# Optimization experiments

Measured on AMD Instinct MI355X. Metric: run time of the kernel, lower is better.

Reference implementation:

```python
import jax, jax.numpy as jnp
import numpy as np

N_NODES = 50000
N_EDGES = 800000
IN_DIM = 128
OUT_DIM = 128
NUM_RELS = 100
NUM_BASES = 4


def setup_inputs() -> dict:
    key = jax.random.key(0)
    ks = jax.random.split(key, 8)
    h = jax.random.normal(ks[0], (N_NODES, IN_DIM), dtype=jnp.float32)
    norm = jax.random.uniform(ks[1], (N_NODES, 1), dtype=jnp.float32)
    src = jax.random.randint(ks[2], (N_EDGES,), 0, N_NODES, dtype=jnp.int32)
    dst = jax.random.randint(ks[3], (N_EDGES,), 0, N_NODES, dtype=jnp.int32)
    rel_type = jax.random.randint(ks[4], (N_EDGES,), 0, NUM_RELS, dtype=jnp.int32)
    basis_weights = jax.random.normal(ks[5], (NUM_BASES, IN_DIM, OUT_DIM), dtype=jnp.float32) * (2.0 / np.sqrt(IN_DIM + OUT_DIM))
    coefficients = jax.random.normal(ks[6], (NUM_RELS, NUM_BASES), dtype=jnp.float32) * (1.0 / np.sqrt(NUM_RELS + NUM_BASES))
    loop_weight = jax.random.normal(ks[7], (IN_DIM, OUT_DIM), dtype=jnp.float32) * (2.0 / np.sqrt(IN_DIM + OUT_DIM))
    return {
        'h': h, 'norm': norm, 'src': src, 'dst': dst, 'rel_type': rel_type,
        'basis_weights': basis_weights, 'coefficients': coefficients,
        'loop_weight': loop_weight,
    }


def reference(h, norm, src, dst, rel_type, basis_weights, coefficients, loop_weight):
    # h: (N, in), norm: (N, 1), src/dst/rel_type: (E,)
    # basis_weights: (B, in, out), coefficients: (R, B), loop_weight: (in, out)
    n_nodes = h.shape[0]
    num_bases = basis_weights.shape[0]

    # self-loop message (dropout=0 -> identity)
    loop_message = h @ loop_weight  # (N, out)

    # W[r] = sum_b coeff[r, b] * basis[b]; per-edge msg_e = h[src_e] @ W[rel_e].
    # Reassociated: project nodes by each basis once, then mix per edge by
    # the relation coefficients -- identical math, avoids the (E, in, out)
    # gathered weight tensor of the original per-edge bmm.
    hb = jnp.einsum('ni,bio->bno', h, basis_weights)  # (B, N, out)
    c_e = coefficients[rel_type]  # (E, B)
    msg = c_e[:, 0, None] * hb[0][src]
    for b in range(1, num_bases):  # small fixed basis count
        msg = msg + c_e[:, b, None] * hb[b][src]  # (E, out)

    # scatter-sum aggregation to destination nodes, then norm scaling
    agg = jax.ops.segment_sum(msg, dst, num_segments=n_nodes)  # (N, out)
    node_repr = agg * norm  # _apply_func
    node_repr = node_repr + loop_message  # self-loop (bias=None)
    return jax.nn.relu(node_repr)  # activation
```

## Files before the change

kernel.cpp:

```cpp
#include <hip/hip_runtime.h>

typedef short bf16x8 __attribute__((ext_vector_type(8)));
typedef float floatx4 __attribute__((ext_vector_type(4)));
typedef float floatx2 __attribute__((ext_vector_type(2)));

typedef const __attribute__((address_space(1))) void* gas_ptr;
typedef __attribute__((address_space(3))) void* las_ptr;

#define EPB  4096
#define MAXB 6144

__device__ __forceinline__ unsigned short f2bf(float f) {
    unsigned int u = __float_as_uint(f);
    unsigned int r = u + 0x7fffu + ((u >> 16) & 1u);
    return (unsigned short)(r >> 16);
}

__device__ __forceinline__ void stage16(const void* g, void* lbase, int lane) {
#if __has_builtin(__builtin_amdgcn_global_load_lds)
    __builtin_amdgcn_global_load_lds((gas_ptr)g, (las_ptr)lbase, 16, 0, 0);
#else
    *(float4*)((char*)lbase + lane * 16) = *(const float4*)g;
#endif
}

__global__ __launch_bounds__(256) void prep_all(
    const float* __restrict__ h, unsigned short* __restrict__ hbf, int nconv,
    const int* __restrict__ dst, int* __restrict__ gh, int E, int nB, int nblkH,
    const float* __restrict__ basis, const float* __restrict__ loopw,
    unsigned short* __restrict__ WT2, int nb_conv)
{
    __shared__ int lh[256];
    const int b = blockIdx.x;
    const int t = threadIdx.x;
    if (b < nb_conv) {
        int idx = b * 256 + t;
        if (idx < nconv) {
            float2 v = *(const float2*)(h + (size_t)idx * 2);
            unsigned int pack = (unsigned int)f2bf(v.x) | ((unsigned int)f2bf(v.y) << 16);
            *(unsigned int*)(hbf + (size_t)idx * 2) = pack;
        }
    } else if (b < nb_conv + nblkH) {
        const int blk = b - nb_conv;
        lh[t] = 0;
        __syncthreads();
        const int cbase = blk * EPB;
#pragma unroll
        for (int j = 0; j < EPB / 256; ++j) {
            int e = cbase + j * 256 + t;
            if (e < E) atomicAdd(&lh[dst[e] >> 8], 1);
        }
        __syncthreads();
        if (t < nB) gh[(size_t)t * nblkH + blk] = lh[t];
    } else {
        int c = b - nb_conv - nblkH;
        for (int k = t; k < 640; k += 256) {
            float v;
            if (k < 512) v = basis[(size_t)k * 128 + c];
            else         v = loopw[(size_t)(k - 512) * 128 + c];
            WT2[(size_t)c * 640 + k] = f2bf(v);
        }
    }
}

__global__ __launch_bounds__(256) void scatter_bkt(
    const int* __restrict__ dst, const int* __restrict__ src,
    const int* __restrict__ rel, const int* __restrict__ gh,
    int* __restrict__ binStart, unsigned int* __restrict__ tmp,
    int E, int nB, int nblkH)
{
    __shared__ int ss[256];
    __shared__ int cur[256];
    const int j = blockIdx.x;
    const int t = threadIdx.x;

    int pre = 0, tot = 0;
    if (t < nB) {
        const int* row = gh + (size_t)t * nblkH;
#pragma unroll 8
        for (int c = 0; c < nblkH; ++c) {
            int v = row[c];
            tot += v;
            if (c < j) pre += v;
        }
    }
    int v = (t < nB) ? tot : 0;
    ss[t] = v;
    __syncthreads();
    for (int o = 1; o < 256; o <<= 1) {
        int x = (t >= o) ? ss[t - o] : 0;
        __syncthreads();
        ss[t] += x;
        __syncthreads();
    }
    const int gstart = ss[t] - v;
    cur[t] = gstart + pre;
    if (j == 0) {
        if (t < nB) binStart[t] = gstart;
        if (t == 0) binStart[nB] = E;
    }
    __syncthreads();

    const int cbase = j * EPB;
#pragma unroll
    for (int jj = 0; jj < EPB / 256; ++jj) {
        int e = cbase + jj * 256 + t;
        if (e < E) {
            int d = dst[e];
            int slot = atomicAdd(&cur[d >> 8], 1);
            tmp[slot] = (unsigned int)src[e] | ((unsigned int)rel[e] << 16)
                      | ((unsigned int)(d & 255) << 23);
        }
    }
}

__global__ __launch_bounds__(256) void bucket_sort(
    const unsigned int* __restrict__ tmp, const int* __restrict__ binStart,
    unsigned int* __restrict__ sedge, int* __restrict__ rowptr,
    int E, int N, int nB)
{
    __shared__ unsigned int eb[MAXB];
    __shared__ int hh[256], ss[256], cur[256];
    const int b = blockIdx.x;
    const int t = threadIdx.x;
    const int brow = binStart[b];
    const int next = binStart[b + 1];
    int n = next - brow;
    if (n > MAXB) n = MAXB;
    hh[t] = 0;
    __syncthreads();
    for (int i = t; i < n; i += 256) {
        unsigned int v = tmp[brow + i];
        eb[i] = v;
        atomicAdd(&hh[(v >> 23) & 255], 1);
    }
    __syncthreads();
    int v = hh[t];
    ss[t] = v;
    __syncthreads();
    for (int o = 1; o < 256; o <<= 1) {
        int x = (t >= o) ? ss[t - o] : 0;
        __syncthreads();
        ss[t] += x;
        __syncthreads();
    }
    const int excl = ss[t] - v;
    const int idx = b * 256 + t;
    if (idx <= N) rowptr[idx] = brow + excl;
    cur[t] = excl;
    __syncthreads();
    for (int i = t; i < n; i += 256) {
        unsigned int e = eb[i];
        int slot = atomicAdd(&cur[(e >> 23) & 255], 1);
        sedge[brow + slot] = ((e & 0xFFFFu) << 8) | (((e >> 16) & 0x7Fu) << 25);
    }
}

__global__ __launch_bounds__(256) void aggregate_pre(
    const unsigned short* __restrict__ hbf,
    const int* __restrict__ rowptr,
    const unsigned int* __restrict__ sedge,
    const float* __restrict__ coeff,
    const float* __restrict__ norm,
    unsigned short* __restrict__ A2, int N, int R)
{
    __shared__ float scoef[512];
    for (int i = threadIdx.x; i < R * 4; i += 256) scoef[i] = coeff[i];
    __syncthreads();

    const int wave = threadIdx.x >> 6;
    const int lane = threadIdx.x & 63;
    const int d = blockIdx.x * 4 + wave;
    if (d >= N) return;
    int i = rowptr[d];
    const int end = rowptr[d + 1];

    const char* hbase = (const char*)hbf + lane * 4;

    floatx2 a0 = {0.f, 0.f}, a1 = {0.f, 0.f}, a2 = {0.f, 0.f}, a3 = {0.f, 0.f};

#define EDGE_LOAD(v, u) \
    unsigned int u = *(const unsigned int*)(hbase + ((v) & 0x00FFFF00u));
#define EDGE_MATH(v, u) { \
    const float4 c = *(const float4*)((const char*)scoef + (((v) >> 25) << 4)); \
    floatx2 hp; \
    hp[0] = __uint_as_float((u) << 16); \
    hp[1] = __uint_as_float((u) & 0xFFFF0000u); \
    a0 = __builtin_elementwise_fma((floatx2){c.x, c.x}, hp, a0); \
    a1 = __builtin_elementwise_fma((floatx2){c.y, c.y}, hp, a1); \
    a2 = __builtin_elementwise_fma((floatx2){c.z, c.z}, hp, a2); \
    a3 = __builtin_elementwise_fma((floatx2){c.w, c.w}, hp, a3); }

    while (i < end && (i & 3)) {
        unsigned int v = sedge[i];
        EDGE_LOAD(v, u)
        EDGE_MATH(v, u)
        ++i;
    }
    for (; i + 8 <= end; i += 8) {
        uint4 e0 = *(const uint4*)(sedge + i);
        uint4 e1 = *(const uint4*)(sedge + i + 4);
        EDGE_LOAD(e0.x, u0) EDGE_LOAD(e0.y, u1) EDGE_LOAD(e0.z, u2) EDGE_LOAD(e0.w, u3)
        EDGE_LOAD(e1.x, u4) EDGE_LOAD(e1.y, u5) EDGE_LOAD(e1.z, u6) EDGE_LOAD(e1.w, u7)
        EDGE_MATH(e0.x, u0) EDGE_MATH(e0.y, u1) EDGE_MATH(e0.z, u2) EDGE_MATH(e0.w, u3)
        EDGE_MATH(e1.x, u4) EDGE_MATH(e1.y, u5) EDGE_MATH(e1.z, u6) EDGE_MATH(e1.w, u7)
    }
    for (; i + 4 <= end; i += 4) {
        uint4 e0 = *(const uint4*)(sedge + i);
        EDGE_LOAD(e0.x, u0) EDGE_LOAD(e0.y, u1) EDGE_LOAD(e0.z, u2) EDGE_LOAD(e0.w, u3)
        EDGE_MATH(e0.x, u0) EDGE_MATH(e0.y, u1) EDGE_MATH(e0.z, u2) EDGE_MATH(e0.w, u3)
    }
    for (; i < end; ++i) {
        unsigned int v = sedge[i];
        EDGE_LOAD(v, u)
        EDGE_MATH(v, u)
    }
#undef EDGE_LOAD
#undef EDGE_MATH

    const float nm = norm[d];
    unsigned short* row = A2 + (size_t)d * 512 + lane * 2;
    *(unsigned int*)(row)       = (unsigned int)f2bf(a0[0] * nm) | ((unsigned int)f2bf(a0[1] * nm) << 16);
    *(unsigned int*)(row + 128) = (unsigned int)f2bf(a1[0] * nm) | ((unsigned int)f2bf(a1[1] * nm) << 16);
    *(unsigned int*)(row + 256) = (unsigned int)f2bf(a2[0] * nm) | ((unsigned int)f2bf(a2[1] * nm) << 16);
    *(unsigned int*)(row + 384) = (unsigned int)f2bf(a3[0] * nm) | ((unsigned int)f2bf(a3[1] * nm) << 16);
}

__global__ __launch_bounds__(256) void final_gemm(
    const unsigned short* __restrict__ A2,
    const unsigned short* __restrict__ hbf,
    const unsigned short* __restrict__ WT2,
    float* __restrict__ out, int N)
{
    __shared__ char sA[16384];
    __shared__ char sB[16384];
    const int t = threadIdx.x;
    const int w = t >> 6;
    const int lane = t & 63;
    const int quad = lane >> 4;
    const int low  = lane & 15;
    const int wr = w >> 1, wc = w & 1;
    const int m0 = blockIdx.x * 128;

    floatx4 acc[4][4];
#pragma unroll
    for (int mt = 0; mt < 4; ++mt)
#pragma unroll
        for (int nt = 0; nt < 4; ++nt) acc[mt][nt] = (floatx4){0.f, 0.f, 0.f, 0.f};

    for (int it = 0; it < 10; ++it) {
        const int k0 = it * 64;
#pragma unroll
        for (int i = 0; i < 4; ++i) {
            const int slot = i * 256 + t;
            const int kc  = slot >> 7;
            const int idx = slot & 127;
            int grow = m0 + idx;
            if (grow >= N) grow = N - 1;
            const unsigned short* gA = (k0 < 512)
                ? A2  + (size_t)grow * 512 + k0 + kc * 8
                : hbf + (size_t)grow * 128 + (k0 - 512) + kc * 8;
            const unsigned short* gB = WT2 + (size_t)idx * 640 + k0 + kc * 8;
            stage16(gA, sA + (size_t)(i * 256 + w * 64) * 16, lane);
            stage16(gB, sB + (size_t)(i * 256 + w * 64) * 16, lane);
        }
        __syncthreads();

#pragma unroll
        for (int ks = 0; ks < 2; ++ks) {
            bf16x8 af[4], bfr[4];
#pragma unroll
            for (int mt = 0; mt < 4; ++mt)
                af[mt] = *(const bf16x8*)(sA + (size_t)(((ks * 4 + quad) << 7) + wr * 64 + mt * 16 + low) * 16);
#pragma unroll
            for (int nt = 0; nt < 4; ++nt)
                bfr[nt] = *(const bf16x8*)(sB + (size_t)(((ks * 4 + quad) << 7) + wc * 64 + nt * 16 + low) * 16);
#pragma unroll
            for (int mt = 0; mt < 4; ++mt)
#pragma unroll
                for (int nt = 0; nt < 4; ++nt)
                    acc[mt][nt] = __builtin_amdgcn_mfma_f32_16x16x32_bf16(af[mt], bfr[nt], acc[mt][nt], 0, 0, 0);
        }
        __syncthreads();
    }

#pragma unroll
    for (int mt = 0; mt < 4; ++mt) {
#pragma unroll
        for (int nt = 0; nt < 4; ++nt) {
            const int c = wc * 64 + nt * 16 + low;
#pragma unroll
            for (int r = 0; r < 4; ++r) {
                int rr = m0 + wr * 64 + mt * 16 + quad * 4 + r;
                if (rr < N) out[(size_t)rr * 128 + c] = fmaxf(acc[mt][nt][r], 0.f);
            }
        }
    }
}

extern "C" void kernel_launch(void* const* d_in, const int* in_sizes, int n_in,
                              void* d_out, int out_size, void* d_ws, size_t ws_size,
                              hipStream_t stream)
{
    const float* h     = (const float*)d_in[0];
    const float* norm  = (const float*)d_in[1];
    const int*   src   = (const int*)d_in[2];
    const int*   dst   = (const int*)d_in[3];
    const int*   rel   = (const int*)d_in[4];
    const float* basis = (const float*)d_in[5];
    const float* coeff = (const float*)d_in[6];
    const float* loopw = (const float*)d_in[7];
    float* out = (float*)d_out;

    const int N = in_sizes[1];
    const int E = in_sizes[2];
    const int R = in_sizes[6] / 4;

    const int nB      = (N + 255) >> 8;
    const int nblkH   = (E + EPB - 1) / EPB;
    const int M       = nB * nblkH;
    const int nb_conv = (N * 64 + 255) / 256;

    char* ws = (char*)d_ws;
    size_t off = 0;
    auto walloc = [&](size_t bytes) -> char* {
        char* p = ws + off;
        off = (off + bytes + 255) & ~(size_t)255;
        return p;
    };
    unsigned short* A2       = (unsigned short*)walloc((size_t)N * 512 * 2);
    unsigned short* hbf      = (unsigned short*)walloc((size_t)N * 128 * 2);
    unsigned short* WT2      = (unsigned short*)walloc(128 * 640 * 2);
    int*            gh       = (int*)walloc((size_t)M * 4);
    int*            binStart = (int*)walloc((size_t)(nB + 1) * 4);
    unsigned int*   tmp      = (unsigned int*)walloc((size_t)E * 4);
    unsigned int*   sedge    = (unsigned int*)walloc((size_t)E * 4);
    int*            rowptr   = (int*)walloc((size_t)(N + 1) * 4);

    prep_all<<<nb_conv + nblkH + 128, 256, 0, stream>>>(
        h, hbf, N * 64, dst, gh, E, nB, nblkH, basis, loopw, WT2, nb_conv);
    scatter_bkt<<<nblkH, 256, 0, stream>>>(dst, src, rel, gh, binStart, tmp, E, nB, nblkH);
    bucket_sort<<<nB, 256, 0, stream>>>(tmp, binStart, sedge, rowptr, E, N, nB);
    aggregate_pre<<<(N + 3) / 4, 256, 0, stream>>>(hbf, rowptr, sedge, coeff, norm, A2, N, R);
    final_gemm<<<(N + 127) / 128, 256, 0, stream>>>(A2, hbf, WT2, out, N);
}
```

Before: 206.7 us.

## Split wave into half-waves per edge in aggregation; shrink GEMM M-tile to 64

The aggregation kernel now has each half-wave (32 lanes) process a different edge and load 8 bytes of the bf16 row per lane, then combines the two halves with a cross-lane shuffle before one half writes. The aim is wider gather loads and twice as many edges in flight per wave instruction. Separately, the final GEMM tile shrinks from 128 to 64 rows, which doubles the number of blocks (about 782 vs 391) to fill more CUs, at the cost of reloading the weight tile more often. The shuffle reduction and the alignment prologue add overhead and branch divergence.

```diff
diff --git a/kernel.cpp b/kernel.cpp
--- a/kernel.cpp
+++ b/kernel.cpp
@@ -170,60 +170,88 @@
 
     const int wave = threadIdx.x >> 6;
     const int lane = threadIdx.x & 63;
+    const int half = lane >> 5;
+    const int l5   = lane & 31;
     const int d = blockIdx.x * 4 + wave;
     if (d >= N) return;
     int i = rowptr[d];
     const int end = rowptr[d + 1];
 
-    const char* hbase = (const char*)hbf + lane * 4;
-
-    floatx2 a0 = {0.f, 0.f}, a1 = {0.f, 0.f}, a2 = {0.f, 0.f}, a3 = {0.f, 0.f};
-
-#define EDGE_LOAD(v, u) \
-    unsigned int u = *(const unsigned int*)(hbase + ((v) & 0x00FFFF00u));
-#define EDGE_MATH(v, u) { \
+    const char* hbase = (const char*)hbf + l5 * 8;
+
+    floatx2 a00 = {0.f,0.f}, a01 = {0.f,0.f}, a10 = {0.f,0.f}, a11 = {0.f,0.f};
+    floatx2 a20 = {0.f,0.f}, a21 = {0.f,0.f}, a30 = {0.f,0.f}, a31 = {0.f,0.f};
+
+#define SLOAD(v, g) uint2 g = *(const uint2*)(hbase + ((v) & 0x00FFFF00u));
+#define SMATH(v, g) { \
     const float4 c = *(const float4*)((const char*)scoef + (((v) >> 25) << 4)); \
-    floatx2 hp; \
-    hp[0] = __uint_as_float((u) << 16); \
-    hp[1] = __uint_as_float((u) & 0xFFFF0000u); \
-    a0 = __builtin_elementwise_fma((floatx2){c.x, c.x}, hp, a0); \
-    a1 = __builtin_elementwise_fma((floatx2){c.y, c.y}, hp, a1); \
-    a2 = __builtin_elementwise_fma((floatx2){c.z, c.z}, hp, a2); \
-    a3 = __builtin_elementwise_fma((floatx2){c.w, c.w}, hp, a3); }
-
-    while (i < end && (i & 3)) {
+    floatx2 h0, h1; \
+    h0[0] = __uint_as_float((g).x << 16); \
+    h0[1] = __uint_as_float((g).x & 0xFFFF0000u); \
+    h1[0] = __uint_as_float((g).y << 16); \
+    h1[1] = __uint_as_float((g).y & 0xFFFF0000u); \
+    a00 = __builtin_elementwise_fma((floatx2){c.x, c.x}, h0, a00); \
+    a01 = __builtin_elementwise_fma((floatx2){c.x, c.x}, h1, a01); \
+    a10 = __builtin_elementwise_fma((floatx2){c.y, c.y}, h0, a10); \
+    a11 = __builtin_elementwise_fma((floatx2){c.y, c.y}, h1, a11); \
+    a20 = __builtin_elementwise_fma((floatx2){c.z, c.z}, h0, a20); \
+    a21 = __builtin_elementwise_fma((floatx2){c.z, c.z}, h1, a21); \
+    a30 = __builtin_elementwise_fma((floatx2){c.w, c.w}, h0, a30); \
+    a31 = __builtin_elementwise_fma((floatx2){c.w, c.w}, h1, a31); }
+
+    if ((i & 1) && i < end) {
+        if (half == 0) {
+            unsigned int v = sedge[i];
+            SLOAD(v, g) SMATH(v, g)
+        }
+        ++i;
+    }
+    if ((i & 2) && i + 2 <= end) {
+        unsigned int v = sedge[i + half];
+        SLOAD(v, g) SMATH(v, g)
+        i += 2;
+    }
+    for (; i + 16 <= end; i += 16) {
+        uint4 w0 = *(const uint4*)(sedge + i + half * 4);
+        uint4 w1 = *(const uint4*)(sedge + i + 8 + half * 4);
+        SLOAD(w0.x, g0) SLOAD(w0.y, g1) SLOAD(w0.z, g2) SLOAD(w0.w, g3)
+        SLOAD(w1.x, g4) SLOAD(w1.y, g5) SLOAD(w1.z, g6) SLOAD(w1.w, g7)
+        SMATH(w0.x, g0) SMATH(w0.y, g1) SMATH(w0.z, g2) SMATH(w0.w, g3)
+        SMATH(w1.x, g4) SMATH(w1.y, g5) SMATH(w1.z, g6) SMATH(w1.w, g7)
+    }
+    for (; i + 2 <= end; i += 2) {
+        unsigned int v = sedge[i + half];
+        SLOAD(v, g) SMATH(v, g)
+    }
+    if (i < end && half == 0) {
         unsigned int v = sedge[i];
-        EDGE_LOAD(v, u)
-        EDGE_MATH(v, u)
-        ++i;
-    }
-    for (; i + 8 <= end; i += 8) {
-        uint4 e0 = *(const uint4*)(sedge + i);
-        uint4 e1 = *(const uint4*)(sedge + i + 4);
-        EDGE_LOAD(e0.x, u0) EDGE_LOAD(e0.y, u1) EDGE_LOAD(e0.z, u2) EDGE_LOAD(e0.w, u3)
-        EDGE_LOAD(e1.x, u4) EDGE_LOAD(e1.y, u5) EDGE_LOAD(e1.z, u6) EDGE_LOAD(e1.w, u7)
-        EDGE_MATH(e0.x, u0) EDGE_MATH(e0.y, u1) EDGE_MATH(e0.z, u2) EDGE_MATH(e0.w, u3)
-        EDGE_MATH(e1.x, u4) EDGE_MATH(e1.y, u5) EDGE_MATH(e1.z, u6) EDGE_MATH(e1.w, u7)
-    }
-    for (; i + 4 <= end; i += 4) {
-        uint4 e0 = *(const uint4*)(sedge + i);
-        EDGE_LOAD(e0.x, u0) EDGE_LOAD(e0.y, u1) EDGE_LOAD(e0.z, u2) EDGE_LOAD(e0.w, u3)
-        EDGE_MATH(e0.x, u0) EDGE_MATH(e0.y, u1) EDGE_MATH(e0.z, u2) EDGE_MATH(e0.w, u3)
-    }
-    for (; i < end; ++i) {
-        unsigned int v = sedge[i];
-        EDGE_LOAD(v, u)
-        EDGE_MATH(v, u)
-    }
-#undef EDGE_LOAD
-#undef EDGE_MATH
-
-    const float nm = norm[d];
-    unsigned short* row = A2 + (size_t)d * 512 + lane * 2;
-    *(unsigned int*)(row)       = (unsigned int)f2bf(a0[0] * nm) | ((unsigned int)f2bf(a0[1] * nm) << 16);
-    *(unsigned int*)(row + 128) = (unsigned int)f2bf(a1[0] * nm) | ((unsigned int)f2bf(a1[1] * nm) << 16);
-    *(unsigned int*)(row + 256) = (unsigned int)f2bf(a2[0] * nm) | ((unsigned int)f2bf(a2[1] * nm) << 16);
-    *(unsigned int*)(row + 384) = (unsigned int)f2bf(a3[0] * nm) | ((unsigned int)f2bf(a3[1] * nm) << 16);
+        SLOAD(v, g) SMATH(v, g)
+    }
+#undef SLOAD
+#undef SMATH
+
+#define COMB(r) { r[0] += __shfl_xor(r[0], 32); r[1] += __shfl_xor(r[1], 32); }
+    COMB(a00) COMB(a01) COMB(a10) COMB(a11)
+    COMB(a20) COMB(a21) COMB(a30) COMB(a31)
+#undef COMB
+
+    if (half == 0) {
+        const float nm = norm[d];
+        unsigned short* row = A2 + (size_t)d * 512 + l5 * 4;
+        uint2 p0, p1, p2, p3;
+        p0.x = (unsigned int)f2bf(a00[0]*nm) | ((unsigned int)f2bf(a00[1]*nm) << 16);
+        p0.y = (unsigned int)f2bf(a01[0]*nm) | ((unsigned int)f2bf(a01[1]*nm) << 16);
+        p1.x = (unsigned int)f2bf(a10[0]*nm) | ((unsigned int)f2bf(a10[1]*nm) << 16);
+        p1.y = (unsigned int)f2bf(a11[0]*nm) | ((unsigned int)f2bf(a11[1]*nm) << 16);
+        p2.x = (unsigned int)f2bf(a20[0]*nm) | ((unsigned int)f2bf(a20[1]*nm) << 16);
+        p2.y = (unsigned int)f2bf(a21[0]*nm) | ((unsigned int)f2bf(a21[1]*nm) << 16);
+        p3.x = (unsigned int)f2bf(a30[0]*nm) | ((unsigned int)f2bf(a30[1]*nm) << 16);
+        p3.y = (unsigned int)f2bf(a31[0]*nm) | ((unsigned int)f2bf(a31[1]*nm) << 16);
+        *(uint2*)(row)       = p0;
+        *(uint2*)(row + 128) = p1;
+        *(uint2*)(row + 256) = p2;
+        *(uint2*)(row + 384) = p3;
+    }
 }
 
 __global__ __launch_bounds__(256) void final_gemm(
@@ -232,7 +260,7 @@
     const unsigned short* __restrict__ WT2,
     float* __restrict__ out, int N)
 {
-    __shared__ char sA[16384];
+    __shared__ char sA[8192];
     __shared__ char sB[16384];
     const int t = threadIdx.x;
     const int w = t >> 6;
@@ -240,43 +268,49 @@
     const int quad = lane >> 4;
     const int low  = lane & 15;
     const int wr = w >> 1, wc = w & 1;
-    const int m0 = blockIdx.x * 128;
-
-    floatx4 acc[4][4];
-#pragma unroll
-    for (int mt = 0; mt < 4; ++mt)
+    const int m0 = blockIdx.x * 64;
+
+    floatx4 acc[2][4];
+#pragma unroll
+    for (int mt = 0; mt < 2; ++mt)
 #pragma unroll
         for (int nt = 0; nt < 4; ++nt) acc[mt][nt] = (floatx4){0.f, 0.f, 0.f, 0.f};
 
     for (int it = 0; it < 10; ++it) {
         const int k0 = it * 64;
 #pragma unroll
-        for (int i = 0; i < 4; ++i) {
+        for (int i = 0; i < 2; ++i) {
             const int slot = i * 256 + t;
-            const int kc  = slot >> 7;
-            const int idx = slot & 127;
+            const int kc  = slot >> 6;
+            const int idx = slot & 63;
             int grow = m0 + idx;
             if (grow >= N) grow = N - 1;
             const unsigned short* gA = (k0 < 512)
                 ? A2  + (size_t)grow * 512 + k0 + kc * 8
                 : hbf + (size_t)grow * 128 + (k0 - 512) + kc * 8;
+            stage16(gA, sA + (size_t)(i * 256 + w * 64) * 16, lane);
+        }
+#pragma unroll
+        for (int i = 0; i < 4; ++i) {
+            const int slot = i * 256 + t;
+            const int kc  = slot >> 7;
+            const int idx = slot & 127;
             const unsigned short* gB = WT2 + (size_t)idx * 640 + k0 + kc * 8;
-            stage16(gA, sA + (size_t)(i * 256 + w * 64) * 16, lane);
             stage16(gB, sB + (size_t)(i * 256 + w * 64) * 16, lane);
         }
         __syncthreads();
 
 #pragma unroll
         for (int ks = 0; ks < 2; ++ks) {
-            bf16x8 af[4], bfr[4];
-#pragma unroll
-            for (int mt = 0; mt < 4; ++mt)
-                af[mt] = *(const bf16x8*)(sA + (size_t)(((ks * 4 + quad) << 7) + wr * 64 + mt * 16 + low) * 16);
+            bf16x8 af[2], bfr[4];
+#pragma unroll
+            for (int mt = 0; mt < 2; ++mt)
+                af[mt] = *(const bf16x8*)(sA + (size_t)(((ks * 4 + quad) << 6) + wr * 32 + mt * 16 + low) * 16);
 #pragma unroll
             for (int nt = 0; nt < 4; ++nt)
                 bfr[nt] = *(const bf16x8*)(sB + (size_t)(((ks * 4 + quad) << 7) + wc * 64 + nt * 16 + low) * 16);
 #pragma unroll
-            for (int mt = 0; mt < 4; ++mt)
+            for (int mt = 0; mt < 2; ++mt)
 #pragma unroll
                 for (int nt = 0; nt < 4; ++nt)
                     acc[mt][nt] = __builtin_amdgcn_mfma_f32_16x16x32_bf16(af[mt], bfr[nt], acc[mt][nt], 0, 0, 0);
@@ -285,13 +319,13 @@
     }
 
 #pragma unroll
-    for (int mt = 0; mt < 4; ++mt) {
+    for (int mt = 0; mt < 2; ++mt) {
 #pragma unroll
         for (int nt = 0; nt < 4; ++nt) {
             const int c = wc * 64 + nt * 16 + low;
 #pragma unroll
             for (int r = 0; r < 4; ++r) {
-                int rr = m0 + wr * 64 + mt * 16 + quad * 4 + r;
+                int rr = m0 + wr * 32 + mt * 16 + quad * 4 + r;
                 if (rr < N) out[(size_t)rr * 128 + c] = fmaxf(acc[mt][nt][r], 0.f);
             }
         }
@@ -342,5 +376,5 @@
     scatter_bkt<<<nblkH, 256, 0, stream>>>(dst, src, rel, gh, binStart, tmp, E, nB, nblkH);
     bucket_sort<<<nB, 256, 0, stream>>>(tmp, binStart, sedge, rowptr, E, N, nB);
     aggregate_pre<<<(N + 3) / 4, 256, 0, stream>>>(hbf, rowptr, sedge, coeff, norm, A2, N, R);
-    final_gemm<<<(N + 127) / 128, 256, 0, stream>>>(A2, hbf, WT2, out, N);
-}
+    final_gemm<<<(N + 63) / 64, 256, 0, stream>>>(A2, hbf, WT2, out, N);
+}
```

After: 224.0 us. +8.4%, slower.
